# Kernel tuning notes

Hardware: AMD Instinct MI355X
Metric: run time of the kernel (lower is better)

## Reference

```python
import jax, jax.numpy as jnp
import numpy as np

NUM_HEADS = 16

def _stablemax3_s(x):
    # 3rd-order Taylor approx of exp(x), Eq 38
    pos = 1.0 + x * (1.0 + 0.5 * x * (1.0 + x / 3.0))
    neg = 1.0 / (1.0 - x * (1.0 - 0.5 * x * (1.0 - x / 3.0)))
    return jnp.where(x >= 0, pos, neg)

def stablemax3(logits, axis=-1):
    logits = logits - jnp.max(logits, axis=axis, keepdims=True)
    s = _stablemax3_s(logits)
    return s / jnp.sum(s, axis=axis, keepdims=True)

def setup_inputs() -> dict:
    key = jax.random.key(0)
    k1, k2, k3 = jax.random.split(key, 3)
    B, S, D = 2, 2048, 1024
    x = jax.random.normal(k1, (B, S, D), dtype=jnp.float32)
    w_qkv = jax.random.normal(k2, (3 * D, D), dtype=jnp.float32) * 0.02
    w_out = jax.random.normal(k3, (D, D), dtype=jnp.float32) * 0.02
    b_out = jnp.zeros((D,), dtype=jnp.float32)
    return {"x": x, "w_qkv": w_qkv, "w_out": w_out, "b_out": b_out}

def reference(x, w_qkv, w_out, b_out):
    B, S, D = x.shape
    H = NUM_HEADS
    hd = D // H
    scale = hd ** (-0.5)
    qkv = x @ w_qkv.T                                  # [B, S, 3D]
    qkv = qkv.reshape(B, S, 3, H, hd)
    qkv = jnp.transpose(qkv, (2, 0, 3, 1, 4))          # [3, B, H, S, hd]
    q, k, v = qkv[0], qkv[1], qkv[2]                   # pos(.) is identity here
    attn = jnp.einsum('bhsd,bhtd->bhst', q, k) * scale # [B, H, S, S]
    attn = stablemax3(attn, axis=-1)
    out = jnp.einsum('bhst,bhtd->bhsd', attn, v)       # [B, H, S, hd]
    out = jnp.transpose(out, (0, 2, 1, 3)).reshape(B, S, D)
    return out @ w_out.T + b_out
```

## Files before the change

kernel.cpp:

```cpp
#include <hip/hip_runtime.h>

typedef _Float16 half8 __attribute__((ext_vector_type(8)));
typedef _Float16 half4 __attribute__((ext_vector_type(4)));
typedef _Float16 half2v __attribute__((ext_vector_type(2)));
typedef float floatx4 __attribute__((ext_vector_type(4)));
typedef unsigned int uint2v __attribute__((ext_vector_type(2)));
typedef unsigned int uint4v __attribute__((ext_vector_type(4)));

__device__ __forceinline__ void gl_lds16(const _Float16* g, _Float16* l) {
    __builtin_amdgcn_global_load_lds(
        (const __attribute__((address_space(1))) void*)g,
        (__attribute__((address_space(3))) void*)l, 16, 0, 0);
}

__device__ __forceinline__ half2v cvt_pk(float a, float b) {
    return __builtin_bit_cast(half2v, __builtin_amdgcn_cvt_pkrtz(a, b));
}

__device__ __forceinline__ half2v rcp2(half2v d) {
#if __has_builtin(__builtin_amdgcn_rcph)
    half2v r;
    r[0] = __builtin_amdgcn_rcph(d[0]);
    r[1] = __builtin_amdgcn_rcph(d[1]);
    return r;
#else
    half2v r;
    r[0] = (_Float16)__builtin_amdgcn_rcpf((float)d[0]);
    r[1] = (_Float16)__builtin_amdgcn_rcpf((float)d[1]);
    return r;
#endif
}

__device__ __forceinline__ float dot2acc(half2v a, float acc) {
#if __has_builtin(__builtin_amdgcn_fdot2)
    const half2v one = {(_Float16)1.0f, (_Float16)1.0f};
    return __builtin_amdgcn_fdot2(a, one, acc, false);
#else
    return acc + (float)a[0] + (float)a[1];
#endif
}

__device__ __forceinline__ half8 from4(half2v a, half2v b, half2v c, half2v d) {
    uint4v u = {__builtin_bit_cast(unsigned int, a), __builtin_bit_cast(unsigned int, b),
                __builtin_bit_cast(unsigned int, c), __builtin_bit_cast(unsigned int, d)};
    return __builtin_bit_cast(half8, u);
}

__device__ __forceinline__ half8 from_lohi(half4 lo, half4 hi) {
    uint2v l = __builtin_bit_cast(uint2v, lo);
    uint2v h = __builtin_bit_cast(uint2v, hi);
    uint4v u = {l[0], l[1], h[0], h[1]};
    return __builtin_bit_cast(half8, u);
}

__global__ __launch_bounds__(256) void cvt_xw(const floatx4* __restrict__ x,
                                              const floatx4* __restrict__ wq,
                                              half4* __restrict__ xh,
                                              half4* __restrict__ wqh) {
    int i = blockIdx.x * 256 + threadIdx.x;
    floatx4 v;
    half4 h;
    if (i < 1048576) {
        v = x[i];
#pragma unroll
        for (int j = 0; j < 4; ++j) h[j] = (_Float16)v[j];
        xh[i] = h;
    } else {
        int j4 = i - 1048576;
        v = wq[j4];
#pragma unroll
        for (int j = 0; j < 4; ++j) h[j] = (_Float16)v[j];
        wqh[j4] = h;
    }
}

__global__ __launch_bounds__(256) void cvt_f32_f16(const floatx4* __restrict__ in,
                                                   half4* __restrict__ out, int n4) {
    int i = blockIdx.x * 256 + threadIdx.x;
    if (i >= n4) return;
    floatx4 v = in[i];
    half4 h;
#pragma unroll
    for (int j = 0; j < 4; ++j) h[j] = (_Float16)v[j];
    out[i] = h;
}

__global__ __launch_bounds__(256) void gemm_qkv(const _Float16* __restrict__ A,
                                                const _Float16* __restrict__ B,
                                                _Float16* __restrict__ qh,
                                                _Float16* __restrict__ kh,
                                                _Float16* __restrict__ vth) {
    const int K = 1024;
    __shared__ _Float16 SH[128 * 68];
    _Float16* As = SH;
    _Float16* Bs = SH + 4096;
    const int t = threadIdx.x;
    const int lane = t & 63, w = t >> 6;
    const int l15 = lane & 15, quad = lane >> 4;
    const int wm = w >> 1, wn = w & 1;
    const int m0 = blockIdx.y * 128, n0 = blockIdx.x * 128;

    floatx4 acc[4][4];
    const floatx4 zf = {0.f, 0.f, 0.f, 0.f};
#pragma unroll
    for (int i = 0; i < 4; ++i)
#pragma unroll
        for (int j = 0; j < 4; ++j) acc[i][j] = zf;

    for (int kt = 0; kt < K; kt += 32) {
        __syncthreads();
#pragma unroll
        for (int it = 0; it < 2; ++it) {
            int cc = it * 256 + t;
            int row = cc >> 2, kc = cc & 3;
            gl_lds16(&A[(size_t)(m0 + row) * K + kt + kc * 8], &As[cc * 8]);
            gl_lds16(&B[(size_t)(n0 + row) * K + kt + kc * 8], &Bs[cc * 8]);
        }
        __syncthreads();
        half8 af[4], bfr[4];
#pragma unroll
        for (int i = 0; i < 4; ++i)
            af[i] = *(const half8*)&As[(wm * 64 + i * 16 + l15) * 32 + quad * 8];
#pragma unroll
        for (int i = 0; i < 4; ++i)
            bfr[i] = *(const half8*)&Bs[(wn * 64 + i * 16 + l15) * 32 + quad * 8];
#pragma unroll
        for (int mi = 0; mi < 4; ++mi)
#pragma unroll
            for (int ni = 0; ni < 4; ++ni)
                acc[mi][ni] = __builtin_amdgcn_mfma_f32_16x16x32_f16(af[mi], bfr[ni],
                                                                     acc[mi][ni], 0, 0, 0);
    }

    const int b = m0 >> 11, s0 = m0 & 2047;
#pragma unroll
    for (int hf = 0; hf < 2; ++hf) {
        __syncthreads();
        if (wn == hf) {
#pragma unroll
            for (int mi = 0; mi < 4; ++mi)
#pragma unroll
                for (int ni = 0; ni < 4; ++ni)
#pragma unroll
                    for (int r = 0; r < 4; ++r)
                        SH[(wm * 64 + mi * 16 + quad * 4 + r) * 68 + ni * 16 + l15] =
                            (_Float16)acc[mi][ni][r];
        }
        __syncthreads();
        const int cbase = n0 + hf * 64;
        if (n0 < 2048) {
            const int hh = (cbase & 1023) >> 6;
            _Float16* dst = (n0 < 1024 ? qh : kh) + (size_t)((b << 4) | hh) * 131072;
#pragma unroll
            for (int it = 0; it < 4; ++it) {
                int cc = it * 256 + t;
                int r = cc >> 3, c8 = cc & 7;
                half4 lo = *(const half4*)&SH[r * 68 + c8 * 8];
                half4 hi = *(const half4*)&SH[r * 68 + c8 * 8 + 4];
                *(half8*)&dst[(size_t)(s0 + r) * 64 + c8 * 8] = from_lohi(lo, hi);
            }
        } else {
            const int hh = (cbase - 2048) >> 6;
            _Float16* dst = vth + (size_t)((b << 4) | hh) * 131072;
#pragma unroll
            for (int it = 0; it < 4; ++it) {
                int cc = it * 256 + t;
                int d = cc >> 4, s8 = cc & 15;
                half8 v;
#pragma unroll
                for (int j = 0; j < 8; ++j) v[j] = SH[(s8 * 8 + j) * 68 + d];
                *(half8*)&dst[(size_t)d * 2048 + s0 + s8 * 8] = v;
            }
        }
    }
}

__global__ __launch_bounds__(256) void gemm_out(const _Float16* __restrict__ A,
                                                const _Float16* __restrict__ B,
                                                float* __restrict__ C,
                                                const float* __restrict__ bias) {
    const int K = 1024, N = 1024;
    __shared__ _Float16 SH[6144];
    _Float16* As = SH;
    _Float16* Bs = SH + 2048;
    const int t = threadIdx.x;
    const int lane = t & 63, w = t >> 6;
    const int l15 = lane & 15, quad = lane >> 4;
    const int wm = w >> 1, wn = w & 1;
    const int m0 = blockIdx.y * 64, n0 = blockIdx.x * 128;

    floatx4 acc[2][4];
    const floatx4 zf = {0.f, 0.f, 0.f, 0.f};
#pragma unroll
    for (int i = 0; i < 2; ++i)
#pragma unroll
        for (int j = 0; j < 4; ++j) acc[i][j] = zf;

    for (int kt = 0; kt < K; kt += 32) {
        __syncthreads();
        {
            int row = t >> 2, kc = t & 3;
            gl_lds16(&A[(size_t)(m0 + row) * K + kt + kc * 8], &As[t * 8]);
        }
#pragma unroll
        for (int it = 0; it < 2; ++it) {
            int cc = it * 256 + t;
            int row = cc >> 2, kc = cc & 3;
            gl_lds16(&B[(size_t)(n0 + row) * K + kt + kc * 8], &Bs[cc * 8]);
        }
        __syncthreads();
        half8 af[2], bfr[4];
#pragma unroll
        for (int i = 0; i < 2; ++i)
            af[i] = *(const half8*)&As[(wm * 32 + i * 16 + l15) * 32 + quad * 8];
#pragma unroll
        for (int i = 0; i < 4; ++i)
            bfr[i] = *(const half8*)&Bs[(wn * 64 + i * 16 + l15) * 32 + quad * 8];
#pragma unroll
        for (int mi = 0; mi < 2; ++mi)
#pragma unroll
            for (int ni = 0; ni < 4; ++ni)
                acc[mi][ni] = __builtin_amdgcn_mfma_f32_16x16x32_f16(af[mi], bfr[ni],
                                                                     acc[mi][ni], 0, 0, 0);
    }

#pragma unroll
    for (int mi = 0; mi < 2; ++mi) {
#pragma unroll
        for (int ni = 0; ni < 4; ++ni) {
            int col = n0 + wn * 64 + ni * 16 + l15;
            float bv = bias[col];
#pragma unroll
            for (int r = 0; r < 4; ++r) {
                int row = m0 + wm * 32 + mi * 16 + quad * 4 + r;
                C[(size_t)row * N + col] = acc[mi][ni][r] + bv;
            }
        }
    }
}

__global__ __launch_bounds__(256) void attn_kernel(const _Float16* __restrict__ qh,
                                                   const _Float16* __restrict__ kh,
                                                   const _Float16* __restrict__ vth,
                                                   _Float16* __restrict__ out) {
    __shared__ _Float16 SM[2 * 64 * 72];
    _Float16* Ks = SM;
    _Float16* VTs = SM + 64 * 72;

    const int t = threadIdx.x;
    const int lane = t & 63, w = t >> 6;
    const int l15 = lane & 15, quad = lane >> 4;
    const int q0 = blockIdx.x * 128;
    const int bh = blockIdx.y;
    const int b = bh >> 4, h = bh & 15;

    const _Float16* Qp = qh + (size_t)bh * 131072 + q0 * 64;
    const _Float16* Kp = kh + (size_t)bh * 131072;
    const _Float16* VTp = vth + (size_t)bh * 131072;

    const floatx4 zf = {0.f, 0.f, 0.f, 0.f};

    half8 qf[2][2];
#pragma unroll
    for (int nh = 0; nh < 2; ++nh)
#pragma unroll
        for (int kk = 0; kk < 2; ++kk) {
            half8 q = *(const half8*)&Qp[(w * 32 + nh * 16 + l15) * 64 + kk * 32 + quad * 8];
#pragma unroll
            for (int j = 0; j < 8; ++j) q[j] = q[j] * (_Float16)0.125f;
            qf[nh][kk] = q;
        }

    float rmax[2] = {-1.0e30f, -1.0e30f};

    for (int kt = 0; kt < 2048; kt += 64) {
        __syncthreads();
#pragma unroll
        for (int it = 0; it < 2; ++it) {
            int cc = it * 256 + t;
            int r = cc >> 3, c8 = cc & 7;
            *(half8*)&Ks[r * 72 + c8 * 8] = *(const half8*)&Kp[kt * 64 + cc * 8];
        }
        __syncthreads();
        floatx4 sa[4][2];
#pragma unroll
        for (int T = 0; T < 4; ++T) { sa[T][0] = zf; sa[T][1] = zf; }
#pragma unroll
        for (int kk = 0; kk < 2; ++kk) {
            half8 kf[4];
#pragma unroll
            for (int T = 0; T < 4; ++T)
                kf[T] = *(const half8*)&Ks[(T * 16 + l15) * 72 + kk * 32 + quad * 8];
#pragma unroll
            for (int T = 0; T < 4; ++T)
#pragma unroll
                for (int nh = 0; nh < 2; ++nh)
                    sa[T][nh] = __builtin_amdgcn_mfma_f32_16x16x32_f16(kf[T], qf[nh][kk],
                                                                      sa[T][nh], 0, 0, 0);
        }
#pragma unroll
        for (int T = 0; T < 4; ++T)
#pragma unroll
            for (int nh = 0; nh < 2; ++nh)
#pragma unroll
                for (int r = 0; r < 4; ++r)
                    rmax[nh] = fmaxf(rmax[nh], sa[T][nh][r]);
    }
#pragma unroll
    for (int nh = 0; nh < 2; ++nh) {
        rmax[nh] = fmaxf(rmax[nh], __shfl_xor(rmax[nh], 16, 64));
        rmax[nh] = fmaxf(rmax[nh], __shfl_xor(rmax[nh], 32, 64));
    }
    const float xm[2] = {-rmax[0], -rmax[1]};

    const half2v cA = {(_Float16)(-1.0f / 6.0f), (_Float16)(-1.0f / 6.0f)};
    const half2v cB = {(_Float16)0.5f, (_Float16)0.5f};
    const half2v cC = {(_Float16)-1.0f, (_Float16)-1.0f};
    const half2v cD = {(_Float16)1.0f, (_Float16)1.0f};

    float rsum[2] = {0.f, 0.f};
    floatx4 oacc[4][2];
#pragma unroll
    for (int i = 0; i < 4; ++i) { oacc[i][0] = zf; oacc[i][1] = zf; }

    for (int kt = 0; kt < 2048; kt += 64) {
        __syncthreads();
#pragma unroll
        for (int it = 0; it < 2; ++it) {
            int cc = it * 256 + t;
            int r = cc >> 3, c8 = cc & 7;
            *(half8*)&Ks[r * 72 + c8 * 8] = *(const half8*)&Kp[kt * 64 + cc * 8];
            *(half8*)&VTs[r * 72 + c8 * 8] =
                *(const half8*)&VTp[(size_t)r * 2048 + kt + c8 * 8];
        }
        __syncthreads();
        floatx4 sa[4][2];
#pragma unroll
        for (int T = 0; T < 4; ++T) { sa[T][0] = zf; sa[T][1] = zf; }
#pragma unroll
        for (int kk = 0; kk < 2; ++kk) {
            half8 kf[4];
#pragma unroll
            for (int T = 0; T < 4; ++T)
                kf[T] = *(const half8*)&Ks[(T * 16 + l15) * 72 + kk * 32 + quad * 8];
#pragma unroll
            for (int T = 0; T < 4; ++T)
#pragma unroll
                for (int nh = 0; nh < 2; ++nh)
                    sa[T][nh] = __builtin_amdgcn_mfma_f32_16x16x32_f16(kf[T], qf[nh][kk],
                                                                      sa[T][nh], 0, 0, 0);
        }
#pragma unroll
        for (int c = 0; c < 2; ++c) {
            half8 vf[4];
#pragma unroll
            for (int di = 0; di < 4; ++di) {
                half4 lo = *(const half4*)&VTs[(di * 16 + l15) * 72 + c * 32 + 4 * quad];
                half4 hi = *(const half4*)&VTs[(di * 16 + l15) * 72 + c * 32 + 16 + 4 * quad];
                vf[di] = from_lohi(lo, hi);
            }
#pragma unroll
            for (int nh = 0; nh < 2; ++nh) {
                half2v p2m[4];
#pragma unroll
                for (int m = 0; m < 4; ++m) {
                    int T = 2 * c + (m >> 1);
                    int r0 = (m & 1) * 2;
                    half2v x2 = cvt_pk(sa[T][nh][r0] + xm[nh],
                                       sa[T][nh][r0 + 1] + xm[nh]);
                    half2v hp = __builtin_elementwise_fma(x2, cA, cB);
                    hp = __builtin_elementwise_fma(x2, hp, cC);
                    hp = __builtin_elementwise_fma(x2, hp, cD);
                    half2v p2 = rcp2(hp);
                    rsum[nh] = dot2acc(p2, rsum[nh]);
                    p2m[m] = p2;
                }
                half8 pb = from4(p2m[0], p2m[1], p2m[2], p2m[3]);
#pragma unroll
                for (int di = 0; di < 4; ++di)
                    oacc[di][nh] = __builtin_amdgcn_mfma_f32_16x16x32_f16(vf[di], pb,
                                                                         oacc[di][nh], 0, 0, 0);
            }
        }
    }

#pragma unroll
    for (int nh = 0; nh < 2; ++nh) {
        rsum[nh] += __shfl_xor(rsum[nh], 16, 64);
        rsum[nh] += __shfl_xor(rsum[nh], 32, 64);
    }
    const float inv[2] = {1.0f / rsum[0], 1.0f / rsum[1]};

    __syncthreads();
    _Float16* Os = SM;
#pragma unroll
    for (int di = 0; di < 4; ++di) {
#pragma unroll
        for (int nh = 0; nh < 2; ++nh) {
            half4 hv;
#pragma unroll
            for (int r = 0; r < 4; ++r) hv[r] = (_Float16)(oacc[di][nh][r] * inv[nh]);
            *(half4*)&Os[(w * 32 + nh * 16 + l15) * 72 + di * 16 + quad * 4] = hv;
        }
    }
    __syncthreads();
    _Float16* Op = out + (size_t)(b * 2048 + q0) * 1024 + h * 64;
#pragma unroll
    for (int it = 0; it < 4; ++it) {
        int cc = it * 256 + t;
        int r = cc >> 3, c8 = cc & 7;
        *(half8*)&Op[(size_t)r * 1024 + c8 * 8] = *(const half8*)&Os[r * 72 + c8 * 8];
    }
}

extern "C" void kernel_launch(void* const* d_in, const int* in_sizes, int n_in,
                              void* d_out, int out_size, void* d_ws, size_t ws_size,
                              hipStream_t stream) {
    const float* x_f = (const float*)d_in[0];
    const float* wqkv_f = (const float*)d_in[1];
    const float* wout_f = (const float*)d_in[2];
    const float* bias_f = (const float*)d_in[3];

    char* ws = (char*)d_ws;
    _Float16* xh = (_Float16*)(ws);
    _Float16* aoh = xh;
    _Float16* wqh = (_Float16*)(ws + 8388608);
    _Float16* woh = wqh;
    _Float16* qh = (_Float16*)(ws + 14680064);
    _Float16* kh = (_Float16*)(ws + 23068672);
    _Float16* vth = (_Float16*)(ws + 31457280);

    cvt_xw<<<7168, 256, 0, stream>>>((const floatx4*)x_f, (const floatx4*)wqkv_f,
                                     (half4*)xh, (half4*)wqh);
    gemm_qkv<<<dim3(24, 32), 256, 0, stream>>>(xh, wqh, qh, kh, vth);
    cvt_f32_f16<<<1024, 256, 0, stream>>>((const floatx4*)wout_f, (half4*)woh, 262144);
    attn_kernel<<<dim3(16, 32), 256, 0, stream>>>(qh, kh, vth, aoh);
    gemm_out<<<dim3(8, 64), 256, 0, stream>>>(aoh, woh, (float*)d_out, bias_f);
}
```

Before: 217.2 us.

## Double-buffer K/V via async global-to-LDS loads with swizzle and 8 waves

Rewrites the attention kernel to use 512 threads (8 waves, 16 query rows each) instead of 4 waves with 32 rows each. K and V^T tiles are now prefetched with async global_load_lds into double-buffered LDS, using an XOR swizzle instead of padded rows to avoid bank conflicts. This overlaps tile loads with MFMA compute and halves per-thread register state for higher occupancy. The cost is more LDS traffic per query row, since each wave reads K/V for fewer rows, plus swizzled address arithmetic.

```diff
diff --git a/kernel.cpp b/kernel.cpp
--- a/kernel.cpp
+++ b/kernel.cpp
@@ -239,17 +239,16 @@
     }
 }
 
-__global__ __launch_bounds__(256) void attn_kernel(const _Float16* __restrict__ qh,
-                                                   const _Float16* __restrict__ kh,
-                                                   const _Float16* __restrict__ vth,
-                                                   _Float16* __restrict__ out) {
-    __shared__ _Float16 SM[2 * 64 * 72];
-    _Float16* Ks = SM;
-    _Float16* VTs = SM + 64 * 72;
+__global__ __launch_bounds__(512, 4) void attn_kernel(const _Float16* __restrict__ qh,
+                                                      const _Float16* __restrict__ kh,
+                                                      const _Float16* __restrict__ vth,
+                                                      _Float16* __restrict__ out) {
+    __shared__ _Float16 SM[16384];
 
     const int t = threadIdx.x;
     const int lane = t & 63, w = t >> 6;
     const int l15 = lane & 15, quad = lane >> 4;
+    const int sw = l15 & 7;
     const int q0 = blockIdx.x * 128;
     const int bh = blockIdx.y;
     const int b = bh >> 4, h = bh & 15;
@@ -258,156 +257,144 @@
     const _Float16* Kp = kh + (size_t)bh * 131072;
     const _Float16* VTp = vth + (size_t)bh * 131072;
 
+    const int srow = t >> 3;
+    const int scg = (t & 7) ^ (srow & 7);
+    const _Float16* Ksrc = &Kp[(size_t)srow * 64 + scg * 8];
+    const _Float16* Vsrc = &VTp[(size_t)srow * 2048 + scg * 8];
+    _Float16* Kdst0 = &SM[t * 8];
+    _Float16* Kdst1 = &SM[4096 + t * 8];
+    _Float16* Vdst0 = &SM[8192 + t * 8];
+    _Float16* Vdst1 = &SM[12288 + t * 8];
+
     const floatx4 zf = {0.f, 0.f, 0.f, 0.f};
 
-    half8 qf[2][2];
-#pragma unroll
-    for (int nh = 0; nh < 2; ++nh)
-#pragma unroll
-        for (int kk = 0; kk < 2; ++kk) {
-            half8 q = *(const half8*)&Qp[(w * 32 + nh * 16 + l15) * 64 + kk * 32 + quad * 8];
-#pragma unroll
-            for (int j = 0; j < 8; ++j) q[j] = q[j] * (_Float16)0.125f;
-            qf[nh][kk] = q;
-        }
-
-    float rmax[2] = {-1.0e30f, -1.0e30f};
-
-    for (int kt = 0; kt < 2048; kt += 64) {
-        __syncthreads();
-#pragma unroll
-        for (int it = 0; it < 2; ++it) {
-            int cc = it * 256 + t;
-            int r = cc >> 3, c8 = cc & 7;
-            *(half8*)&Ks[r * 72 + c8 * 8] = *(const half8*)&Kp[kt * 64 + cc * 8];
-        }
-        __syncthreads();
-        floatx4 sa[4][2];
-#pragma unroll
-        for (int T = 0; T < 4; ++T) { sa[T][0] = zf; sa[T][1] = zf; }
+    half8 qf[2];
+#pragma unroll
+    for (int kk = 0; kk < 2; ++kk) {
+        half8 q = *(const half8*)&Qp[(w * 16 + l15) * 64 + kk * 32 + quad * 8];
+#pragma unroll
+        for (int j = 0; j < 8; ++j) q[j] = q[j] * (_Float16)0.125f;
+        qf[kk] = q;
+    }
+
+    float rmax = -1.0e30f;
+    gl_lds16(Ksrc, Kdst0);
+    __syncthreads();
+    for (int kt = 0, cur = 0; kt < 2048; kt += 64, cur ^= 1) {
+        if (kt + 64 < 2048)
+            gl_lds16(Ksrc + (size_t)(kt + 64) * 64, cur ? Kdst0 : Kdst1);
+        const _Float16* Ks = cur ? &SM[4096] : &SM[0];
+        floatx4 sa[4];
+#pragma unroll
+        for (int T = 0; T < 4; ++T) sa[T] = zf;
 #pragma unroll
         for (int kk = 0; kk < 2; ++kk) {
             half8 kf[4];
 #pragma unroll
             for (int T = 0; T < 4; ++T)
-                kf[T] = *(const half8*)&Ks[(T * 16 + l15) * 72 + kk * 32 + quad * 8];
+                kf[T] = *(const half8*)&Ks[((T * 16 + l15) << 6) +
+                                           ((((kk << 2) + quad) ^ sw) << 3)];
 #pragma unroll
             for (int T = 0; T < 4; ++T)
-#pragma unroll
-                for (int nh = 0; nh < 2; ++nh)
-                    sa[T][nh] = __builtin_amdgcn_mfma_f32_16x16x32_f16(kf[T], qf[nh][kk],
-                                                                      sa[T][nh], 0, 0, 0);
+                sa[T] = __builtin_amdgcn_mfma_f32_16x16x32_f16(kf[T], qf[kk], sa[T], 0, 0, 0);
         }
 #pragma unroll
         for (int T = 0; T < 4; ++T)
 #pragma unroll
-            for (int nh = 0; nh < 2; ++nh)
-#pragma unroll
-                for (int r = 0; r < 4; ++r)
-                    rmax[nh] = fmaxf(rmax[nh], sa[T][nh][r]);
-    }
-#pragma unroll
-    for (int nh = 0; nh < 2; ++nh) {
-        rmax[nh] = fmaxf(rmax[nh], __shfl_xor(rmax[nh], 16, 64));
-        rmax[nh] = fmaxf(rmax[nh], __shfl_xor(rmax[nh], 32, 64));
-    }
-    const float xm[2] = {-rmax[0], -rmax[1]};
+            for (int r = 0; r < 4; ++r)
+                rmax = fmaxf(rmax, sa[T][r]);
+        __syncthreads();
+    }
+    rmax = fmaxf(rmax, __shfl_xor(rmax, 16, 64));
+    rmax = fmaxf(rmax, __shfl_xor(rmax, 32, 64));
+    const float xm = -rmax;
 
     const half2v cA = {(_Float16)(-1.0f / 6.0f), (_Float16)(-1.0f / 6.0f)};
     const half2v cB = {(_Float16)0.5f, (_Float16)0.5f};
     const half2v cC = {(_Float16)-1.0f, (_Float16)-1.0f};
     const half2v cD = {(_Float16)1.0f, (_Float16)1.0f};
 
-    float rsum[2] = {0.f, 0.f};
-    floatx4 oacc[4][2];
-#pragma unroll
-    for (int i = 0; i < 4; ++i) { oacc[i][0] = zf; oacc[i][1] = zf; }
-
-    for (int kt = 0; kt < 2048; kt += 64) {
-        __syncthreads();
-#pragma unroll
-        for (int it = 0; it < 2; ++it) {
-            int cc = it * 256 + t;
-            int r = cc >> 3, c8 = cc & 7;
-            *(half8*)&Ks[r * 72 + c8 * 8] = *(const half8*)&Kp[kt * 64 + cc * 8];
-            *(half8*)&VTs[r * 72 + c8 * 8] =
-                *(const half8*)&VTp[(size_t)r * 2048 + kt + c8 * 8];
-        }
-        __syncthreads();
-        floatx4 sa[4][2];
-#pragma unroll
-        for (int T = 0; T < 4; ++T) { sa[T][0] = zf; sa[T][1] = zf; }
+    float rsum = 0.f;
+    floatx4 oacc[4];
+#pragma unroll
+    for (int i = 0; i < 4; ++i) oacc[i] = zf;
+
+    gl_lds16(Ksrc, Kdst0);
+    gl_lds16(Vsrc, Vdst0);
+    __syncthreads();
+    for (int kt = 0, cur = 0; kt < 2048; kt += 64, cur ^= 1) {
+        if (kt + 64 < 2048) {
+            gl_lds16(Ksrc + (size_t)(kt + 64) * 64, cur ? Kdst0 : Kdst1);
+            gl_lds16(Vsrc + (kt + 64), cur ? Vdst0 : Vdst1);
+        }
+        const _Float16* Ks = cur ? &SM[4096] : &SM[0];
+        const _Float16* VTs = cur ? &SM[12288] : &SM[8192];
+
+        floatx4 sa[4];
+#pragma unroll
+        for (int T = 0; T < 4; ++T) sa[T] = zf;
 #pragma unroll
         for (int kk = 0; kk < 2; ++kk) {
             half8 kf[4];
 #pragma unroll
             for (int T = 0; T < 4; ++T)
-                kf[T] = *(const half8*)&Ks[(T * 16 + l15) * 72 + kk * 32 + quad * 8];
+                kf[T] = *(const half8*)&Ks[((T * 16 + l15) << 6) +
+                                           ((((kk << 2) + quad) ^ sw) << 3)];
 #pragma unroll
             for (int T = 0; T < 4; ++T)
-#pragma unroll
-                for (int nh = 0; nh < 2; ++nh)
-                    sa[T][nh] = __builtin_amdgcn_mfma_f32_16x16x32_f16(kf[T], qf[nh][kk],
-                                                                      sa[T][nh], 0, 0, 0);
+                sa[T] = __builtin_amdgcn_mfma_f32_16x16x32_f16(kf[T], qf[kk], sa[T], 0, 0, 0);
         }
 #pragma unroll
         for (int c = 0; c < 2; ++c) {
             half8 vf[4];
 #pragma unroll
             for (int di = 0; di < 4; ++di) {
-                half4 lo = *(const half4*)&VTs[(di * 16 + l15) * 72 + c * 32 + 4 * quad];
-                half4 hi = *(const half4*)&VTs[(di * 16 + l15) * 72 + c * 32 + 16 + 4 * quad];
+                const int bl = (di * 16 + l15) << 6;
+                const int clo = (((c << 2) + (quad >> 1)) ^ sw) << 3;
+                const int chi = (((c << 2) + 2 + (quad >> 1)) ^ sw) << 3;
+                half4 lo = *(const half4*)&VTs[bl + clo + ((quad & 1) << 2)];
+                half4 hi = *(const half4*)&VTs[bl + chi + ((quad & 1) << 2)];
                 vf[di] = from_lohi(lo, hi);
             }
-#pragma unroll
-            for (int nh = 0; nh < 2; ++nh) {
-                half2v p2m[4];
-#pragma unroll
-                for (int m = 0; m < 4; ++m) {
-                    int T = 2 * c + (m >> 1);
-                    int r0 = (m & 1) * 2;
-                    half2v x2 = cvt_pk(sa[T][nh][r0] + xm[nh],
-                                       sa[T][nh][r0 + 1] + xm[nh]);
-                    half2v hp = __builtin_elementwise_fma(x2, cA, cB);
-                    hp = __builtin_elementwise_fma(x2, hp, cC);
-                    hp = __builtin_elementwise_fma(x2, hp, cD);
-                    half2v p2 = rcp2(hp);
-                    rsum[nh] = dot2acc(p2, rsum[nh]);
-                    p2m[m] = p2;
-                }
-                half8 pb = from4(p2m[0], p2m[1], p2m[2], p2m[3]);
-#pragma unroll
-                for (int di = 0; di < 4; ++di)
-                    oacc[di][nh] = __builtin_amdgcn_mfma_f32_16x16x32_f16(vf[di], pb,
-                                                                         oacc[di][nh], 0, 0, 0);
+            half2v p2m[4];
+#pragma unroll
+            for (int m = 0; m < 4; ++m) {
+                int T = 2 * c + (m >> 1);
+                int r0 = (m & 1) * 2;
+                half2v x2 = cvt_pk(sa[T][r0] + xm, sa[T][r0 + 1] + xm);
+                half2v hp = __builtin_elementwise_fma(x2, cA, cB);
+                hp = __builtin_elementwise_fma(x2, hp, cC);
+                hp = __builtin_elementwise_fma(x2, hp, cD);
+                half2v p2 = rcp2(hp);
+                rsum = dot2acc(p2, rsum);
+                p2m[m] = p2;
             }
-        }
-    }
-
-#pragma unroll
-    for (int nh = 0; nh < 2; ++nh) {
-        rsum[nh] += __shfl_xor(rsum[nh], 16, 64);
-        rsum[nh] += __shfl_xor(rsum[nh], 32, 64);
-    }
-    const float inv[2] = {1.0f / rsum[0], 1.0f / rsum[1]};
-
-    __syncthreads();
+            half8 pb = from4(p2m[0], p2m[1], p2m[2], p2m[3]);
+#pragma unroll
+            for (int di = 0; di < 4; ++di)
+                oacc[di] = __builtin_amdgcn_mfma_f32_16x16x32_f16(vf[di], pb,
+                                                                 oacc[di], 0, 0, 0);
+        }
+        __syncthreads();
+    }
+
+    rsum += __shfl_xor(rsum, 16, 64);
+    rsum += __shfl_xor(rsum, 32, 64);
+    const float inv = 1.0f / rsum;
+
     _Float16* Os = SM;
 #pragma unroll
     for (int di = 0; di < 4; ++di) {
-#pragma unroll
-        for (int nh = 0; nh < 2; ++nh) {
-            half4 hv;
-#pragma unroll
-            for (int r = 0; r < 4; ++r) hv[r] = (_Float16)(oacc[di][nh][r] * inv[nh]);
-            *(half4*)&Os[(w * 32 + nh * 16 + l15) * 72 + di * 16 + quad * 4] = hv;
-        }
+        half4 hv;
+#pragma unroll
+        for (int r = 0; r < 4; ++r) hv[r] = (_Float16)(oacc[di][r] * inv);
+        *(half4*)&Os[(w * 16 + l15) * 72 + di * 16 + quad * 4] = hv;
     }
     __syncthreads();
     _Float16* Op = out + (size_t)(b * 2048 + q0) * 1024 + h * 64;
 #pragma unroll
-    for (int it = 0; it < 4; ++it) {
-        int cc = it * 256 + t;
+    for (int it = 0; it < 2; ++it) {
+        int cc = it * 512 + t;
         int r = cc >> 3, c8 = cc & 7;
         *(half8*)&Op[(size_t)r * 1024 + c8 * 8] = *(const half8*)&Os[r * 72 + c8 * 8];
     }
@@ -434,6 +421,6 @@
                                      (half4*)xh, (half4*)wqh);
     gemm_qkv<<<dim3(24, 32), 256, 0, stream>>>(xh, wqh, qh, kh, vth);
     cvt_f32_f16<<<1024, 256, 0, stream>>>((const floatx4*)wout_f, (half4*)woh, 262144);
-    attn_kernel<<<dim3(16, 32), 256, 0, stream>>>(qh, kh, vth, aoh);
+    attn_kernel<<<dim3(16, 32), 512, 0, stream>>>(qh, kh, vth, aoh);
     gemm_out<<<dim3(8, 64), 256, 0, stream>>>(aoh, woh, (float*)d_out, bias_f);
 }
```

Result: faster. 211.7 us (-2.5%).

## Double-buffer K/V tiles via async global-to-LDS loads with XOR swizzle

Applied to the files above, without the earlier changes.

Both attention passes now prefetch the next K (and V^T) tile straight into a second LDS buffer with global_load_lds while the current tile is consumed. This leaves one barrier per iteration instead of two and hides global-memory latency behind the MFMA work. The padded LDS layout is replaced by an XOR swizzle on 8-element column groups to avoid bank conflicts. The row-max subtraction is folded into the score accumulator initialisation, and s_setprio is raised around the MFMA blocks. LDS use grows to 32 KB, which may lower occupancy.

```diff
diff --git a/kernel.cpp b/kernel.cpp
--- a/kernel.cpp
+++ b/kernel.cpp
@@ -243,13 +243,12 @@
                                                    const _Float16* __restrict__ kh,
                                                    const _Float16* __restrict__ vth,
                                                    _Float16* __restrict__ out) {
-    __shared__ _Float16 SM[2 * 64 * 72];
-    _Float16* Ks = SM;
-    _Float16* VTs = SM + 64 * 72;
+    __shared__ _Float16 SM[16384];
 
     const int t = threadIdx.x;
     const int lane = t & 63, w = t >> 6;
     const int l15 = lane & 15, quad = lane >> 4;
+    const int sw = l15 & 7;
     const int q0 = blockIdx.x * 128;
     const int bh = blockIdx.y;
     const int b = bh >> 4, h = bh & 15;
@@ -258,6 +257,13 @@
     const _Float16* Kp = kh + (size_t)bh * 131072;
     const _Float16* VTp = vth + (size_t)bh * 131072;
 
+    const int row0 = t >> 3, cg0 = (t & 7) ^ (row0 & 7);
+    const int row1 = 32 + row0, cg1 = (t & 7) ^ (row1 & 7);
+    const _Float16* K0 = &Kp[(size_t)row0 * 64 + cg0 * 8];
+    const _Float16* K1 = &Kp[(size_t)row1 * 64 + cg1 * 8];
+    const _Float16* V0 = &VTp[(size_t)row0 * 2048 + cg0 * 8];
+    const _Float16* V1 = &VTp[(size_t)row1 * 2048 + cg1 * 8];
+
     const floatx4 zf = {0.f, 0.f, 0.f, 0.f};
 
     half8 qf[2][2];
@@ -272,16 +278,16 @@
         }
 
     float rmax[2] = {-1.0e30f, -1.0e30f};
-
-    for (int kt = 0; kt < 2048; kt += 64) {
-        __syncthreads();
-#pragma unroll
-        for (int it = 0; it < 2; ++it) {
-            int cc = it * 256 + t;
-            int r = cc >> 3, c8 = cc & 7;
-            *(half8*)&Ks[r * 72 + c8 * 8] = *(const half8*)&Kp[kt * 64 + cc * 8];
-        }
-        __syncthreads();
+    gl_lds16(K0, &SM[t * 8]);
+    gl_lds16(K1, &SM[2048 + t * 8]);
+    __syncthreads();
+    for (int kt = 0, cur = 0; kt < 2048; kt += 64, cur ^= 1) {
+        if (kt + 64 < 2048) {
+            _Float16* kd = cur ? &SM[0] : &SM[4096];
+            gl_lds16(K0 + (size_t)(kt + 64) * 64, kd + t * 8);
+            gl_lds16(K1 + (size_t)(kt + 64) * 64, kd + 2048 + t * 8);
+        }
+        const _Float16* Ks = cur ? &SM[4096] : &SM[0];
         floatx4 sa[4][2];
 #pragma unroll
         for (int T = 0; T < 4; ++T) { sa[T][0] = zf; sa[T][1] = zf; }
@@ -290,13 +296,16 @@
             half8 kf[4];
 #pragma unroll
             for (int T = 0; T < 4; ++T)
-                kf[T] = *(const half8*)&Ks[(T * 16 + l15) * 72 + kk * 32 + quad * 8];
+                kf[T] = *(const half8*)&Ks[((T * 16 + l15) << 6) +
+                                           ((((kk << 2) + quad) ^ sw) << 3)];
+            __builtin_amdgcn_s_setprio(1);
 #pragma unroll
             for (int T = 0; T < 4; ++T)
 #pragma unroll
                 for (int nh = 0; nh < 2; ++nh)
                     sa[T][nh] = __builtin_amdgcn_mfma_f32_16x16x32_f16(kf[T], qf[nh][kk],
                                                                       sa[T][nh], 0, 0, 0);
+            __builtin_amdgcn_s_setprio(0);
         }
 #pragma unroll
         for (int T = 0; T < 4; ++T)
@@ -305,13 +314,15 @@
 #pragma unroll
                 for (int r = 0; r < 4; ++r)
                     rmax[nh] = fmaxf(rmax[nh], sa[T][nh][r]);
+        __syncthreads();
     }
 #pragma unroll
     for (int nh = 0; nh < 2; ++nh) {
         rmax[nh] = fmaxf(rmax[nh], __shfl_xor(rmax[nh], 16, 64));
         rmax[nh] = fmaxf(rmax[nh], __shfl_xor(rmax[nh], 32, 64));
     }
-    const float xm[2] = {-rmax[0], -rmax[1]};
+    const floatx4 xmv[2] = {{-rmax[0], -rmax[0], -rmax[0], -rmax[0]},
+                            {-rmax[1], -rmax[1], -rmax[1], -rmax[1]}};
 
     const half2v cA = {(_Float16)(-1.0f / 6.0f), (_Float16)(-1.0f / 6.0f)};
     const half2v cB = {(_Float16)0.5f, (_Float16)0.5f};
@@ -323,40 +334,52 @@
 #pragma unroll
     for (int i = 0; i < 4; ++i) { oacc[i][0] = zf; oacc[i][1] = zf; }
 
-    for (int kt = 0; kt < 2048; kt += 64) {
-        __syncthreads();
-#pragma unroll
-        for (int it = 0; it < 2; ++it) {
-            int cc = it * 256 + t;
-            int r = cc >> 3, c8 = cc & 7;
-            *(half8*)&Ks[r * 72 + c8 * 8] = *(const half8*)&Kp[kt * 64 + cc * 8];
-            *(half8*)&VTs[r * 72 + c8 * 8] =
-                *(const half8*)&VTp[(size_t)r * 2048 + kt + c8 * 8];
-        }
-        __syncthreads();
+    gl_lds16(K0, &SM[t * 8]);
+    gl_lds16(K1, &SM[2048 + t * 8]);
+    gl_lds16(V0, &SM[8192 + t * 8]);
+    gl_lds16(V1, &SM[8192 + 2048 + t * 8]);
+    __syncthreads();
+    for (int kt = 0, cur = 0; kt < 2048; kt += 64, cur ^= 1) {
+        if (kt + 64 < 2048) {
+            _Float16* kd = cur ? &SM[0] : &SM[4096];
+            _Float16* vd = cur ? &SM[8192] : &SM[12288];
+            gl_lds16(K0 + (size_t)(kt + 64) * 64, kd + t * 8);
+            gl_lds16(K1 + (size_t)(kt + 64) * 64, kd + 2048 + t * 8);
+            gl_lds16(V0 + (kt + 64), vd + t * 8);
+            gl_lds16(V1 + (kt + 64), vd + 2048 + t * 8);
+        }
+        const _Float16* Ks = cur ? &SM[4096] : &SM[0];
+        const _Float16* VTs = cur ? &SM[12288] : &SM[8192];
+
         floatx4 sa[4][2];
 #pragma unroll
-        for (int T = 0; T < 4; ++T) { sa[T][0] = zf; sa[T][1] = zf; }
+        for (int T = 0; T < 4; ++T) { sa[T][0] = xmv[0]; sa[T][1] = xmv[1]; }
 #pragma unroll
         for (int kk = 0; kk < 2; ++kk) {
             half8 kf[4];
 #pragma unroll
             for (int T = 0; T < 4; ++T)
-                kf[T] = *(const half8*)&Ks[(T * 16 + l15) * 72 + kk * 32 + quad * 8];
+                kf[T] = *(const half8*)&Ks[((T * 16 + l15) << 6) +
+                                           ((((kk << 2) + quad) ^ sw) << 3)];
+            __builtin_amdgcn_s_setprio(1);
 #pragma unroll
             for (int T = 0; T < 4; ++T)
 #pragma unroll
                 for (int nh = 0; nh < 2; ++nh)
                     sa[T][nh] = __builtin_amdgcn_mfma_f32_16x16x32_f16(kf[T], qf[nh][kk],
                                                                       sa[T][nh], 0, 0, 0);
+            __builtin_amdgcn_s_setprio(0);
         }
 #pragma unroll
         for (int c = 0; c < 2; ++c) {
             half8 vf[4];
 #pragma unroll
             for (int di = 0; di < 4; ++di) {
-                half4 lo = *(const half4*)&VTs[(di * 16 + l15) * 72 + c * 32 + 4 * quad];
-                half4 hi = *(const half4*)&VTs[(di * 16 + l15) * 72 + c * 32 + 16 + 4 * quad];
+                const int bl = (di * 16 + l15) << 6;
+                const int clo = (((c << 2) + (quad >> 1)) ^ sw) << 3;
+                const int chi = (((c << 2) + 2 + (quad >> 1)) ^ sw) << 3;
+                half4 lo = *(const half4*)&VTs[bl + clo + ((quad & 1) << 2)];
+                half4 hi = *(const half4*)&VTs[bl + chi + ((quad & 1) << 2)];
                 vf[di] = from_lohi(lo, hi);
             }
 #pragma unroll
@@ -366,8 +389,7 @@
                 for (int m = 0; m < 4; ++m) {
                     int T = 2 * c + (m >> 1);
                     int r0 = (m & 1) * 2;
-                    half2v x2 = cvt_pk(sa[T][nh][r0] + xm[nh],
-                                       sa[T][nh][r0 + 1] + xm[nh]);
+                    half2v x2 = cvt_pk(sa[T][nh][r0], sa[T][nh][r0 + 1]);
                     half2v hp = __builtin_elementwise_fma(x2, cA, cB);
                     hp = __builtin_elementwise_fma(x2, hp, cC);
                     hp = __builtin_elementwise_fma(x2, hp, cD);
@@ -376,12 +398,15 @@
                     p2m[m] = p2;
                 }
                 half8 pb = from4(p2m[0], p2m[1], p2m[2], p2m[3]);
+                __builtin_amdgcn_s_setprio(1);
 #pragma unroll
                 for (int di = 0; di < 4; ++di)
                     oacc[di][nh] = __builtin_amdgcn_mfma_f32_16x16x32_f16(vf[di], pb,
                                                                          oacc[di][nh], 0, 0, 0);
+                __builtin_amdgcn_s_setprio(0);
             }
         }
+        __syncthreads();
     }
 
 #pragma unroll
@@ -391,7 +416,6 @@
     }
     const float inv[2] = {1.0f / rsum[0], 1.0f / rsum[1]};
 
-    __syncthreads();
     _Float16* Os = SM;
 #pragma unroll
     for (int di = 0; di < 4; ++di) {
```

Result: no change. 213.7 us (-1.6%).
